# Optimization experiments

Hardware: AMD Instinct MI355X
Metric: run time of the kernel (lower is better)

The kernel has to match this reference:

```python
import jax, jax.numpy as jnp
import numpy as np
import math

N, T, V, D, DIN, H, L, F, MAXLEN = 8, 512, 32000, 512, 1024, 8, 2, 2048, 512
HD = D // H
STD = 0.02


def setup_inputs() -> dict:
    key = jax.random.key(0)
    ks = jax.random.split(key, 16)
    ln = jnp.stack([jnp.ones((L, D)), jnp.zeros((L, D))], axis=1)  # [L,2,D] (gamma, beta)
    return {
        "features": jax.random.normal(ks[0], (N, DIN), jnp.float32),
        "captions": jax.random.randint(ks[1], (N, T), 0, V, jnp.int32),
        "emb_table": jax.random.normal(ks[2], (V, D), jnp.float32) * STD,
        "pos_table": jax.random.normal(ks[3], (MAXLEN, D), jnp.float32) * STD,
        "feat_W": jax.random.normal(ks[4], (DIN, D), jnp.float32) * STD,
        "feat_b": jnp.zeros((D,), jnp.float32),
        "sa_qkv_W": jax.random.normal(ks[5], (L, 3, D, D), jnp.float32) * STD,
        "sa_qkv_b": jnp.zeros((L, 3, D), jnp.float32),
        "sa_o_W": jax.random.normal(ks[6], (L, D, D), jnp.float32) * STD,
        "sa_o_b": jnp.zeros((L, D), jnp.float32),
        "sa_ln": ln,
        "ca_qkv_W": jax.random.normal(ks[7], (L, 3, D, D), jnp.float32) * STD,
        "ca_qkv_b": jnp.zeros((L, 3, D), jnp.float32),
        "ca_o_W": jax.random.normal(ks[8], (L, D, D), jnp.float32) * STD,
        "ca_o_b": jnp.zeros((L, D), jnp.float32),
        "ca_ln": ln,
        "ff_W1": jax.random.normal(ks[9], (L, D, F), jnp.float32) * STD,
        "ff_b1": jnp.zeros((L, F), jnp.float32),
        "ff_W2": jax.random.normal(ks[10], (L, F, D), jnp.float32) * STD,
        "ff_b2": jnp.zeros((L, D), jnp.float32),
        "ff_ln": ln,
        "out_W": jax.random.normal(ks[11], (D, V), jnp.float32) * STD,
        "out_b": jnp.zeros((V,), jnp.float32),
    }


def layernorm(x, g, b, eps=1e-5):
    mu = jnp.mean(x, axis=-1, keepdims=True)
    var = jnp.mean(jnp.square(x - mu), axis=-1, keepdims=True)
    return (x - mu) * jax.lax.rsqrt(var + eps) * g + b


def mha(xq, xkv, Wqkv, bqkv, Wo, bo, mask):
    # xq: [N,Tq,D], xkv: [N,S,D]; heads split after separate q/k/v projections
    q = xq @ Wqkv[0] + bqkv[0]
    k = xkv @ Wqkv[1] + bqkv[1]
    v = xkv @ Wqkv[2] + bqkv[2]
    q = q.reshape(q.shape[0], q.shape[1], H, HD).transpose(0, 2, 1, 3)  # [N,H,Tq,hd]
    k = k.reshape(k.shape[0], k.shape[1], H, HD).transpose(0, 2, 1, 3)
    v = v.reshape(v.shape[0], v.shape[1], H, HD).transpose(0, 2, 1, 3)
    scores = jnp.einsum("nhtd,nhsd->nhts", q, k) / math.sqrt(HD)
    if mask is not None:
        scores = scores + jnp.where(mask == 0, -jnp.inf, 0.0)  # additive -inf mask
    attn = jax.nn.softmax(scores, axis=-1)  # dropout is identity in eval
    y = jnp.einsum("nhts,nhsd->nhtd", attn, v)
    y = y.transpose(0, 2, 1, 3).reshape(y.shape[0], -1, D)  # [N,Tq,D]
    return y @ Wo + bo


def reference(features, captions, emb_table, pos_table, feat_W, feat_b,
              sa_qkv_W, sa_qkv_b, sa_o_W, sa_o_b, sa_ln,
              ca_qkv_W, ca_qkv_b, ca_o_W, ca_o_b, ca_ln,
              ff_W1, ff_b1, ff_W2, ff_b2, ff_ln, out_W, out_b):
    cond = (features @ feat_W + feat_b)[:, None, :]  # [N,1,D]
    t = captions.shape[1]
    x = emb_table[captions] + pos_table[:t]  # token + positional embedding
    mask = jnp.tril(jnp.ones((t, t), jnp.float32))  # causal mask
    for l in range(L):
        a = mha(x, x, sa_qkv_W[l], sa_qkv_b[l], sa_o_W[l], sa_o_b[l], mask)
        x = layernorm(x + a, sa_ln[l, 0], sa_ln[l, 1])
        a = mha(x, cond, ca_qkv_W[l], ca_qkv_b[l], ca_o_W[l], ca_o_b[l], None)
        x = layernorm(x + a, ca_ln[l, 0], ca_ln[l, 1])
        h = jax.nn.relu(x @ ff_W1[l] + ff_b1[l]) @ ff_W2[l] + ff_b2[l]
        x = layernorm(x + h, ff_ln[l, 0], ff_ln[l, 1])
    return x @ out_W + out_b  # [N,T,V]
```

## Files before the change

### kernel.cpp

```cpp
#include <hip/hip_runtime.h>
#include <math.h>
#include <stdint.h>

#define N_ 8
#define T_ 512
#define V_ 32000
#define D_ 512
#define DIN_ 1024
#define H_ 8
#define HD_ 64
#define L_ 2
#define F_ 2048

typedef __attribute__((ext_vector_type(8))) short short8;
typedef __attribute__((ext_vector_type(4))) float f32x4;

__device__ __forceinline__ short f2bf(float f) {
  uint32_t u = __builtin_bit_cast(uint32_t, f);
  u = (u + 0x7FFFu + ((u >> 16) & 1u)) >> 16;
  return (short)u;
}
__device__ __forceinline__ uint32_t pack_bf2(float a, float b) {
  return (uint32_t)(uint16_t)f2bf(a) | ((uint32_t)(uint16_t)f2bf(b) << 16);
}
__device__ __forceinline__ float bflo(uint32_t u) {
  return __builtin_bit_cast(float, u << 16);
}
__device__ __forceinline__ float bfhi(uint32_t u) {
  return __builtin_bit_cast(float, u & 0xffff0000u);
}
__device__ __forceinline__ void unp8(uint4 p, float* v) {
  v[0] = bflo(p.x); v[1] = bfhi(p.x); v[2] = bflo(p.y); v[3] = bfhi(p.y);
  v[4] = bflo(p.z); v[5] = bfhi(p.z); v[6] = bflo(p.w); v[7] = bfhi(p.w);
}
__device__ __forceinline__ int swzb(int row, int byteoff) {
  return row * 128 + (byteoff ^ ((row & 7) << 4));
}

__global__ __launch_bounds__(256) void batched_transpose_kernel(
    const float* __restrict__ sa_qkv_W, const float* __restrict__ sa_o_W,
    const float* __restrict__ ff_W1, const float* __restrict__ ff_W2,
    const float* __restrict__ out_W, short* __restrict__ wq,
    short* __restrict__ wo, short* __restrict__ w1, short* __restrict__ w2,
    short* __restrict__ outWt) {
  __shared__ float tile[64][65];
  const int t = blockIdx.x;
  const float* src;
  short* dst;
  int K, N, rem;
  if (t < 384) {
    int mat = t >> 6;
    rem = t & 63;
    K = D_; N = D_;
    src = sa_qkv_W + (size_t)mat * D_ * D_;
    dst = wq + (size_t)mat * D_ * D_;
  } else if (t < 512) {
    int lt = t - 384, mat = lt >> 6;
    rem = lt & 63;
    K = D_; N = D_;
    src = sa_o_W + (size_t)mat * D_ * D_;
    dst = wo + (size_t)mat * D_ * D_;
  } else if (t < 1024) {
    int lt = t - 512, mat = lt >> 8;
    rem = lt & 255;
    K = D_; N = F_;
    src = ff_W1 + (size_t)mat * D_ * F_;
    dst = w1 + (size_t)mat * F_ * D_;
  } else if (t < 1536) {
    int lt = t - 1024, mat = lt >> 8;
    rem = lt & 255;
    K = F_; N = D_;
    src = ff_W2 + (size_t)mat * F_ * D_;
    dst = w2 + (size_t)mat * D_ * F_;
  } else {
    rem = t - 1536;
    K = D_; N = V_;
    src = out_W;
    dst = outWt;
  }
  const int nx = N >> 6;
  const int n0 = (rem % nx) * 64, k0 = (rem / nx) * 64;
  const int tid = threadIdx.x;
  const int c = tid & 63, r4 = tid >> 6;
#pragma unroll
  for (int i = 0; i < 16; ++i) {
    int k = r4 + i * 4;
    tile[k][c] = src[(size_t)(k0 + k) * N + n0 + c];
  }
  __syncthreads();
#pragma unroll
  for (int i = 0; i < 16; ++i) {
    int n = r4 + i * 4;
    dst[(size_t)(n0 + n) * K + k0 + c] = f2bf(tile[c][n]);
  }
}

template <int BM, int BN, bool RELU, bool OUTBF, int ORDER, bool NT>
__global__ __launch_bounds__((BM / 64) * (BN / 64) * 64) void bf16_gemm_kernel(
    const short* __restrict__ A, const short* __restrict__ Bt,
    const float* __restrict__ bias, void* __restrict__ Cv, int M, int N,
    int K) {
  constexpr int WM = BM / 64, WN = BN / 64, NW = WM * WN;
  constexpr int AISS = BM / (NW * 8), BISS = BN / (NW * 8);
  __shared__ short As[BM * 64];
  __shared__ short Bs[BN * 64];
  const int tid = threadIdx.x, lane = tid & 63, w = tid >> 6;
  const int wr = w / WN, wc = w % WN;
  const int lhi = lane >> 4, llo = lane & 15;

  const int gx = gridDim.x, gy = gridDim.y;
  const int nwg = gx * gy;
  int lin = blockIdx.y * gx + blockIdx.x;
  if ((nwg & 7) == 0) lin = (lin & 7) * (nwg >> 3) + (lin >> 3);
  int bm, bn;
  if (ORDER == 1) {
    bm = (lin % gy) * BM;
    bn = (lin / gy) * BN;
  } else {
    bm = (lin / gx) * BM;
    bn = (lin % gx) * BN;
  }

  const int arow = lane >> 3;
  const int achunk = ((lane & 7) ^ (lane >> 3)) * 8;

  f32x4 acc[4][4];
#pragma unroll
  for (int i = 0; i < 4; ++i)
#pragma unroll
    for (int j = 0; j < 4; ++j) acc[i][j] = (f32x4)0.f;

  char* AsB = (char*)As;
  char* BsB = (char*)Bs;

  for (int k0 = 0; k0 < K; k0 += 64) {
#pragma unroll
    for (int g = 0; g < AISS; ++g) {
      const int r0 = (w * AISS + g) * 8;
      const short* gp = A + (size_t)(bm + r0 + arow) * K + k0 + achunk;
      __builtin_amdgcn_global_load_lds(
          (const __attribute__((address_space(1))) void*)gp,
          (__attribute__((address_space(3))) void*)&As[r0 * 64], 16, 0, 0);
    }
#pragma unroll
    for (int g = 0; g < BISS; ++g) {
      const int r0 = (w * BISS + g) * 8;
      const short* gp = Bt + (size_t)(bn + r0 + arow) * K + k0 + achunk;
      __builtin_amdgcn_global_load_lds(
          (const __attribute__((address_space(1))) void*)gp,
          (__attribute__((address_space(3))) void*)&Bs[r0 * 64], 16, 0, 0);
    }
    __syncthreads();
#pragma unroll
    for (int ks = 0; ks < 2; ++ks) {
      short8 af[4], bf[4];
#pragma unroll
      for (int i = 0; i < 4; ++i)
        af[i] = *(const short8*)(AsB + swzb(wr * 64 + i * 16 + llo,
                                            ks * 64 + lhi * 16));
#pragma unroll
      for (int j = 0; j < 4; ++j)
        bf[j] = *(const short8*)(BsB + swzb(wc * 64 + j * 16 + llo,
                                            ks * 64 + lhi * 16));
#pragma unroll
      for (int i = 0; i < 4; ++i)
#pragma unroll
        for (int j = 0; j < 4; ++j)
          acc[i][j] = __builtin_amdgcn_mfma_f32_16x16x32_bf16(af[i], bf[j],
                                                              acc[i][j], 0, 0, 0);
    }
    __syncthreads();
  }
#pragma unroll
  for (int j = 0; j < 4; ++j) {
    const int col = bn + wc * 64 + j * 16 + llo;
    const float bv = bias ? bias[col] : 0.f;
#pragma unroll
    for (int i = 0; i < 4; ++i) {
      const int row0 = bm + wr * 64 + i * 16 + lhi * 4;
#pragma unroll
      for (int r = 0; r < 4; ++r) {
        float v = acc[i][j][r] + bv;
        if (RELU) v = fmaxf(v, 0.f);
        if (OUTBF) {
          ((short*)Cv)[(size_t)(row0 + r) * N + col] = f2bf(v);
        } else if (NT) {
          __builtin_nontemporal_store(v, &((float*)Cv)[(size_t)(row0 + r) * N + col]);
        } else {
          ((float*)Cv)[(size_t)(row0 + r) * N + col] = v;
        }
      }
    }
  }
}

template <int BM, int BN, int BK, int TM, int TN>
__global__ __launch_bounds__((BM / TM) * (BN / TN)) void gemm_f32_kernel(
    const short* __restrict__ A, const float* __restrict__ B,
    const float* __restrict__ bias, float* __restrict__ C, int M, int N,
    int K) {
  constexpr int THREADS = (BM / TM) * (BN / TN);
  __shared__ float As[BK][BM + 1];
  __shared__ float Bs[BK][BN + 1];
  const int tid = threadIdx.x;
  const int bm = blockIdx.y * BM, bn = blockIdx.x * BN;
  const int tcol = tid % (BN / TN), trow = tid / (BN / TN);
  float acc[TM][TN];
#pragma unroll
  for (int i = 0; i < TM; ++i)
#pragma unroll
    for (int j = 0; j < TN; ++j) acc[i][j] = 0.f;
  for (int k0 = 0; k0 < K; k0 += BK) {
    for (int i = tid; i < BM * BK; i += THREADS) {
      int m = i / BK, kk = i % BK;
      As[kk][m] = bflo((uint32_t)(uint16_t)A[(size_t)(bm + m) * K + (k0 + kk)]);
    }
    for (int i = tid; i < BK * BN; i += THREADS) {
      int kk = i / BN, n = i % BN;
      Bs[kk][n] = B[(size_t)(k0 + kk) * N + (bn + n)];
    }
    __syncthreads();
#pragma unroll
    for (int kk = 0; kk < BK; ++kk) {
      float a[TM], b[TN];
#pragma unroll
      for (int i = 0; i < TM; ++i) a[i] = As[kk][trow * TM + i];
#pragma unroll
      for (int j = 0; j < TN; ++j) b[j] = Bs[kk][tcol * TN + j];
#pragma unroll
      for (int i = 0; i < TM; ++i)
#pragma unroll
        for (int j = 0; j < TN; ++j) acc[i][j] += a[i] * b[j];
    }
    __syncthreads();
  }
#pragma unroll
  for (int i = 0; i < TM; ++i) {
    int m = bm + trow * TM + i;
#pragma unroll
    for (int j = 0; j < TN; ++j) {
      int n = bn + tcol * TN + j;
      C[(size_t)m * N + n] = acc[i][j] + (bias ? bias[n] : 0.f);
    }
  }
}

__global__ __launch_bounds__(256) void embed_kernel(
    const int* __restrict__ captions, const float* __restrict__ emb,
    const float* __restrict__ pos, short* __restrict__ xb) {
  int idx4 = (blockIdx.x * 256 + threadIdx.x) * 4;
  int d = idx4 % D_;
  int nt = idx4 / D_;
  int t = nt % T_;
  int tok = captions[nt];
  float4 e = *(const float4*)(emb + (size_t)tok * D_ + d);
  float4 p = *(const float4*)(pos + (size_t)t * D_ + d);
  *(uint32_t*)(xb + idx4) = pack_bf2(e.x + p.x, e.y + p.y);
  *(uint32_t*)(xb + idx4 + 2) = pack_bf2(e.z + p.z, e.w + p.w);
}

__global__ __launch_bounds__(256) void wave_mm_kernel(
    const float* __restrict__ A, const float* __restrict__ W,
    const float* __restrict__ bias, float* __restrict__ out, int M, int K,
    int N) {
  const int widx = blockIdx.x * 4 + (threadIdx.x >> 6);
  const int lane = threadIdx.x & 63;
  if (widx >= M * N) return;
  const int m = widx / N, n = widx % N;
  const float* a = A + (size_t)m * K;
  const float* w = W + n;
  float s = 0.f;
  for (int k = lane; k < K; k += 64) s += a[k] * w[(size_t)k * N];
#pragma unroll
  for (int off = 32; off; off >>= 1) s += __shfl_xor(s, off);
  if (lane == 0) out[widx] = s + (bias ? bias[n] : 0.f);
}

__global__ __launch_bounds__(256) void ca_mm_kernel(
    const float* __restrict__ A, size_t a_lstride, const float* __restrict__ W,
    size_t w_lstride, const float* __restrict__ bias, size_t b_lstride,
    float* __restrict__ out, int M, int K, int N) {
  const int widx = blockIdx.x * 4 + (threadIdx.x >> 6);
  const int lane = threadIdx.x & 63;
  if (widx >= L_ * M * N) return;
  const int l = widx / (M * N);
  const int r = widx % (M * N);
  const int m = r / N, n = r % N;
  const float* a = A + l * a_lstride + (size_t)m * K;
  const float* w = W + l * w_lstride + n;
  float s = 0.f;
  for (int k = lane; k < K; k += 64) s += a[k] * w[(size_t)k * N];
#pragma unroll
  for (int off = 32; off; off >>= 1) s += __shfl_xor(s, off);
  if (lane == 0) out[widx] = s + bias[l * b_lstride + n];
}

__global__ __launch_bounds__(256) void flash_attn_kernel(
    const short* __restrict__ qkv, short* __restrict__ y) {
  __shared__ short Ks[2][64 * 64];
  __shared__ short Vt[2][64 * 64];
  __shared__ short Ps[4][16 * 64];
  const int b = blockIdx.x;
  const int pair = b & 255, half = b >> 8;
  const int n = pair >> 5;
  const int h = (pair >> 2) & 7;
  const int tp = pair & 3;
  const int tile = half ? 7 - tp : tp;
  const int t0 = tile * 64;
  const int tid = threadIdx.x, lane = tid & 63, w = tid >> 6;
  const int lhi = lane >> 4, llo = lane & 15;
  char* PsB = (char*)Ps[w];

  const short* qrow = qkv + (size_t)(n * T_ + t0 + w * 16 + llo) * 1536 + h * 64;
  short8 qf[2];
#pragma unroll
  for (int kc = 0; kc < 2; ++kc) qf[kc] = *(const short8*)(qrow + kc * 32 + lhi * 8);

  float m = -1e30f, l = 0.f;
  f32x4 acc[4];
#pragma unroll
  for (int dc = 0; dc < 4; ++dc) acc[dc] = (f32x4)0.f;

  const int arow = lane >> 3;
  const int achunk = ((lane & 7) ^ (lane >> 3)) * 8;
  const int vr = tid >> 2, vd0 = (tid & 3) * 16;
  const int tg = t0 + w * 16 + llo;

  auto stageK = [&](int buf, int s0) {
#pragma unroll
    for (int g = 0; g < 2; ++g) {
      const int r0 = w * 16 + g * 8;
      const short* gp =
          qkv + (size_t)(n * T_ + s0 + r0 + arow) * 1536 + 512 + h * 64 + achunk;
      __builtin_amdgcn_global_load_lds(
          (const __attribute__((address_space(1))) void*)gp,
          (__attribute__((address_space(3))) void*)&Ks[buf][r0 * 64], 16, 0, 0);
    }
  };
  auto loadV = [&](int s0, short8& a, short8& bb) {
    const short* vg = qkv + (size_t)(n * T_ + s0 + vr) * 1536 + 1024 + h * 64 + vd0;
    a = *(const short8*)(vg);
    bb = *(const short8*)(vg + 8);
  };
  auto scatterV = [&](int buf, const short8& a, const short8& bb) {
    char* VtB = (char*)Vt[buf];
#pragma unroll
    for (int j = 0; j < 8; ++j) {
      *(short*)(VtB + swzb(vd0 + j, vr * 2)) = a[j];
      *(short*)(VtB + swzb(vd0 + 8 + j, vr * 2)) = bb[j];
    }
  };

  const int nchunk = tile + 1;
  {
    short8 va, vb;
    stageK(0, 0);
    loadV(0, va, vb);
    scatterV(0, va, vb);
  }
  __syncthreads();

  for (int c = 0; c < nchunk; ++c) {
    const int cur = c & 1;
    const int s0 = c * 64;
    short8 va, vb;
    const bool nxt = (c + 1 < nchunk);
    if (nxt) {
      stageK(cur ^ 1, s0 + 64);
      loadV(s0 + 64, va, vb);
    }
    char* KsB = (char*)Ks[cur];
    char* VtB = (char*)Vt[cur];

    f32x4 st[4];
    __builtin_amdgcn_s_setprio(1);
#pragma unroll
    for (int tle = 0; tle < 4; ++tle) {
      st[tle] = (f32x4)0.f;
#pragma unroll
      for (int kc = 0; kc < 2; ++kc) {
        short8 kf =
            *(const short8*)(KsB + swzb(tle * 16 + llo, kc * 64 + lhi * 16));
        st[tle] =
            __builtin_amdgcn_mfma_f32_16x16x32_bf16(kf, qf[kc], st[tle], 0, 0, 0);
      }
    }
    __builtin_amdgcn_s_setprio(0);
#pragma unroll
    for (int tle = 0; tle < 4; ++tle)
#pragma unroll
      for (int r = 0; r < 4; ++r) st[tle][r] *= 0.125f;
    if (s0 == t0) {
#pragma unroll
      for (int tle = 0; tle < 4; ++tle)
#pragma unroll
        for (int r = 0; r < 4; ++r)
          if (s0 + tle * 16 + lhi * 4 + r > tg) st[tle][r] = -1e30f;
    }
    float cmax = -1e30f;
#pragma unroll
    for (int tle = 0; tle < 4; ++tle)
#pragma unroll
      for (int r = 0; r < 4; ++r) cmax = fmaxf(cmax, st[tle][r]);
    cmax = fmaxf(cmax, __shfl_xor(cmax, 16));
    cmax = fmaxf(cmax, __shfl_xor(cmax, 32));
    float mn = fmaxf(m, cmax);
    float corr = __expf(m - mn);
    float lsum = 0.f;
#pragma unroll
    for (int tle = 0; tle < 4; ++tle)
#pragma unroll
      for (int r = 0; r < 4; ++r) {
        float p = __expf(st[tle][r] - mn);
        st[tle][r] = p;
        lsum += p;
      }
    lsum += __shfl_xor(lsum, 16);
    lsum += __shfl_xor(lsum, 32);
    l = l * corr + lsum;
    m = mn;
#pragma unroll
    for (int tle = 0; tle < 4; ++tle) {
      int base = swzb(llo, tle * 32 + lhi * 8);
      *(uint32_t*)(PsB + base) = pack_bf2(st[tle][0], st[tle][1]);
      *(uint32_t*)(PsB + base + 4) = pack_bf2(st[tle][2], st[tle][3]);
    }
    float c0 = __shfl(corr, lhi * 4 + 0), c1 = __shfl(corr, lhi * 4 + 1);
    float c2 = __shfl(corr, lhi * 4 + 2), c3 = __shfl(corr, lhi * 4 + 3);
#pragma unroll
    for (int dc = 0; dc < 4; ++dc) {
      acc[dc][0] *= c0;
      acc[dc][1] *= c1;
      acc[dc][2] *= c2;
      acc[dc][3] *= c3;
    }
    short8 pf0 = *(const short8*)(PsB + swzb(llo, lhi * 16));
    short8 pf1 = *(const short8*)(PsB + swzb(llo, 64 + lhi * 16));
    __builtin_amdgcn_s_setprio(1);
#pragma unroll
    for (int dc = 0; dc < 4; ++dc) {
      short8 vf0 = *(const short8*)(VtB + swzb(dc * 16 + llo, lhi * 16));
      short8 vf1 = *(const short8*)(VtB + swzb(dc * 16 + llo, 64 + lhi * 16));
      acc[dc] = __builtin_amdgcn_mfma_f32_16x16x32_bf16(pf0, vf0, acc[dc], 0, 0, 0);
      acc[dc] = __builtin_amdgcn_mfma_f32_16x16x32_bf16(pf1, vf1, acc[dc], 0, 0, 0);
    }
    __builtin_amdgcn_s_setprio(0);
    if (nxt) scatterV(cur ^ 1, va, vb);
    __syncthreads();
  }

  float linv = 1.f / l;
  float l0 = __shfl(linv, lhi * 4 + 0), l1 = __shfl(linv, lhi * 4 + 1);
  float l2 = __shfl(linv, lhi * 4 + 2), l3 = __shfl(linv, lhi * 4 + 3);
  short* yb = y + (size_t)(n * T_ + t0 + w * 16) * D_ + h * 64;
#pragma unroll
  for (int dc = 0; dc < 4; ++dc) {
    yb[(size_t)(lhi * 4 + 0) * D_ + dc * 16 + llo] = f2bf(acc[dc][0] * l0);
    yb[(size_t)(lhi * 4 + 1) * D_ + dc * 16 + llo] = f2bf(acc[dc][1] * l1);
    yb[(size_t)(lhi * 4 + 2) * D_ + dc * 16 + llo] = f2bf(acc[dc][2] * l2);
    yb[(size_t)(lhi * 4 + 3) * D_ + dc * 16 + llo] = f2bf(acc[dc][3] * l3);
  }
}

__global__ __launch_bounds__(256) void ln_res_kernel(
    short* __restrict__ xb, const short* __restrict__ res,
    const float* __restrict__ g, const float* __restrict__ b) {
  const int row = blockIdx.x * 4 + (threadIdx.x >> 6);
  const int lane = threadIdx.x & 63;
  const int d0 = lane * 8;
  uint4 xp = *(const uint4*)(xb + (size_t)row * D_ + d0);
  uint4 rp = *(const uint4*)(res + (size_t)row * D_ + d0);
  float xv[8], rv[8], v[8];
  unp8(xp, xv);
  unp8(rp, rv);
  float s = 0.f, sq = 0.f;
#pragma unroll
  for (int i = 0; i < 8; ++i) {
    v[i] = xv[i] + rv[i];
    s += v[i];
    sq += v[i] * v[i];
  }
#pragma unroll
  for (int off = 32; off; off >>= 1) {
    s += __shfl_xor(s, off);
    sq += __shfl_xor(sq, off);
  }
  float mu = s * (1.f / D_);
  float var = sq * (1.f / D_) - mu * mu;
  float r = rsqrtf(var + 1e-5f);
  float4 g0 = *(const float4*)(g + d0), g1 = *(const float4*)(g + d0 + 4);
  float4 b0 = *(const float4*)(b + d0), b1 = *(const float4*)(b + d0 + 4);
  float gg[8] = {g0.x, g0.y, g0.z, g0.w, g1.x, g1.y, g1.z, g1.w};
  float bb[8] = {b0.x, b0.y, b0.z, b0.w, b1.x, b1.y, b1.z, b1.w};
  float o[8];
#pragma unroll
  for (int i = 0; i < 8; ++i) o[i] = (v[i] - mu) * r * gg[i] + bb[i];
  uint4 op = {pack_bf2(o[0], o[1]), pack_bf2(o[2], o[3]),
              pack_bf2(o[4], o[5]), pack_bf2(o[6], o[7])};
  *(uint4*)(xb + (size_t)row * D_ + d0) = op;
}

__global__ __launch_bounds__(256) void ln2_res_kernel(
    short* __restrict__ xb, const short* __restrict__ res,
    const float* __restrict__ oc, const float* __restrict__ g1,
    const float* __restrict__ b1, const float* __restrict__ g2,
    const float* __restrict__ b2) {
  const int row = blockIdx.x * 4 + (threadIdx.x >> 6);
  const int lane = threadIdx.x & 63;
  const int d0 = lane * 8;
  uint4 xp = *(const uint4*)(xb + (size_t)row * D_ + d0);
  uint4 rp = *(const uint4*)(res + (size_t)row * D_ + d0);
  float xv[8], rv[8], v[8];
  unp8(xp, xv);
  unp8(rp, rv);
  float s = 0.f, sq = 0.f;
#pragma unroll
  for (int i = 0; i < 8; ++i) {
    v[i] = xv[i] + rv[i];
    s += v[i];
    sq += v[i] * v[i];
  }
#pragma unroll
  for (int off = 32; off; off >>= 1) {
    s += __shfl_xor(s, off);
    sq += __shfl_xor(sq, off);
  }
  float mu = s * (1.f / D_);
  float var = sq * (1.f / D_) - mu * mu;
  float r = rsqrtf(var + 1e-5f);
  float4 ga = *(const float4*)(g1 + d0), gb = *(const float4*)(g1 + d0 + 4);
  float4 ba = *(const float4*)(b1 + d0), bbv = *(const float4*)(b1 + d0 + 4);
  const float* ocr = oc + (size_t)(row / T_) * D_ + d0;
  float4 oa = *(const float4*)(ocr), ob = *(const float4*)(ocr + 4);
  float g1v[8] = {ga.x, ga.y, ga.z, ga.w, gb.x, gb.y, gb.z, gb.w};
  float b1v[8] = {ba.x, ba.y, ba.z, ba.w, bbv.x, bbv.y, bbv.z, bbv.w};
  float ov[8] = {oa.x, oa.y, oa.z, oa.w, ob.x, ob.y, ob.z, ob.w};
  float u[8];
  float s2 = 0.f, sq2 = 0.f;
#pragma unroll
  for (int i = 0; i < 8; ++i) {
    u[i] = (v[i] - mu) * r * g1v[i] + b1v[i] + ov[i];
    s2 += u[i];
    sq2 += u[i] * u[i];
  }
#pragma unroll
  for (int off = 32; off; off >>= 1) {
    s2 += __shfl_xor(s2, off);
    sq2 += __shfl_xor(sq2, off);
  }
  float mu2 = s2 * (1.f / D_);
  float var2 = sq2 * (1.f / D_) - mu2 * mu2;
  float r2 = rsqrtf(var2 + 1e-5f);
  float4 gc = *(const float4*)(g2 + d0), gd = *(const float4*)(g2 + d0 + 4);
  float4 bc = *(const float4*)(b2 + d0), bd = *(const float4*)(b2 + d0 + 4);
  float g2v[8] = {gc.x, gc.y, gc.z, gc.w, gd.x, gd.y, gd.z, gd.w};
  float b2v[8] = {bc.x, bc.y, bc.z, bc.w, bd.x, bd.y, bd.z, bd.w};
  float o[8];
#pragma unroll
  for (int i = 0; i < 8; ++i) o[i] = (u[i] - mu2) * r2 * g2v[i] + b2v[i];
  uint4 op = {pack_bf2(o[0], o[1]), pack_bf2(o[2], o[3]),
              pack_bf2(o[4], o[5]), pack_bf2(o[6], o[7])};
  *(uint4*)(xb + (size_t)row * D_ + d0) = op;
}

extern "C" void kernel_launch(void* const* d_in, const int* in_sizes, int n_in,
                              void* d_out, int out_size, void* d_ws,
                              size_t ws_size, hipStream_t stream) {
  const float* features = (const float*)d_in[0];
  const int* captions = (const int*)d_in[1];
  const float* emb_table = (const float*)d_in[2];
  const float* pos_table = (const float*)d_in[3];
  const float* feat_W = (const float*)d_in[4];
  const float* feat_b = (const float*)d_in[5];
  const float* sa_qkv_W = (const float*)d_in[6];
  const float* sa_qkv_b = (const float*)d_in[7];
  const float* sa_o_W = (const float*)d_in[8];
  const float* sa_o_b = (const float*)d_in[9];
  const float* sa_ln = (const float*)d_in[10];
  const float* ca_qkv_W = (const float*)d_in[11];
  const float* ca_qkv_b = (const float*)d_in[12];
  const float* ca_o_W = (const float*)d_in[13];
  const float* ca_o_b = (const float*)d_in[14];
  const float* ca_ln = (const float*)d_in[15];
  const float* ff_W1 = (const float*)d_in[16];
  const float* ff_b1 = (const float*)d_in[17];
  const float* ff_W2 = (const float*)d_in[18];
  const float* ff_b2 = (const float*)d_in[19];
  const float* ff_ln = (const float*)d_in[20];
  const float* out_W = (const float*)d_in[21];
  const float* out_b = (const float*)d_in[22];

  const int ROWS = N_ * T_;
  float* out = (float*)d_out;

  short* xb = (short*)d_ws;
  float* cond = (float*)(xb + (size_t)ROWS * D_);
  float* vcAll = cond + N_ * D_;
  float* ocAll = vcAll + (size_t)L_ * N_ * D_;
  short* outWt = (short*)(ocAll + (size_t)L_ * N_ * D_);
  size_t ws_need = (size_t)ROWS * D_ * 2 + (1 + 2 * L_) * N_ * D_ * 4 +
                   (size_t)V_ * D_ * 2;
  const bool big_ws = ws_size >= ws_need;

  short* qkvb = (short*)out;
  short* yb = qkvb + (size_t)ROWS * 3 * D_;
  short* ffhb = yb + (size_t)ROWS * D_;
  short* tmpb = ffhb + (size_t)ROWS * F_;
  short* wq = tmpb + (size_t)ROWS * D_;
  short* wo = wq + (size_t)L_ * 3 * D_ * D_;
  short* w1 = wo + (size_t)L_ * D_ * D_;
  short* w2 = w1 + (size_t)L_ * F_ * D_;

  hipLaunchKernelGGL(batched_transpose_kernel, dim3(big_ws ? 5536 : 1536),
                     dim3(256), 0, stream, sa_qkv_W, sa_o_W, ff_W1, ff_W2,
                     out_W, wq, wo, w1, w2, outWt);

  auto mg128 = [&](const short* A, const short* Bt, const float* bias, void* C,
                   int M, int Nn, int K, bool relu) {
    dim3 grid(Nn / 128, M / 128);
    if (relu)
      hipLaunchKernelGGL((bf16_gemm_kernel<128, 128, true, true, 0, false>),
                         grid, dim3(256), 0, stream, A, Bt, bias, C, M, Nn, K);
    else
      hipLaunchKernelGGL((bf16_gemm_kernel<128, 128, false, true, 0, false>),
                         grid, dim3(256), 0, stream, A, Bt, bias, C, M, Nn, K);
  };
  auto mg64 = [&](const short* A, const short* Bt, const float* bias, void* C,
                  int M, int Nn, int K) {
    dim3 grid(Nn / 128, M / 64);
    hipLaunchKernelGGL((bf16_gemm_kernel<64, 128, false, true, 0, false>),
                       grid, dim3(128), 0, stream, A, Bt, bias, C, M, Nn, K);
  };

  hipLaunchKernelGGL(wave_mm_kernel, dim3((N_ * D_ + 3) / 4), dim3(256), 0,
                     stream, features, feat_W, feat_b, cond, N_, DIN_, D_);
  hipLaunchKernelGGL(ca_mm_kernel, dim3((L_ * N_ * D_ + 3) / 4), dim3(256), 0,
                     stream, cond, (size_t)0, ca_qkv_W + (size_t)2 * D_ * D_,
                     (size_t)3 * D_ * D_, ca_qkv_b + 2 * D_, (size_t)3 * D_,
                     vcAll, N_, D_, D_);
  hipLaunchKernelGGL(ca_mm_kernel, dim3((L_ * N_ * D_ + 3) / 4), dim3(256), 0,
                     stream, vcAll, (size_t)N_ * D_, ca_o_W, (size_t)D_ * D_,
                     ca_o_b, (size_t)D_, ocAll, N_, D_, D_);
  hipLaunchKernelGGL(embed_kernel, dim3(ROWS * D_ / 1024), dim3(256), 0, stream,
                     captions, emb_table, pos_table, xb);

  for (int l = 0; l < L_; ++l) {
    mg128(xb, wq + (size_t)l * 3 * D_ * D_, sa_qkv_b + (size_t)l * 3 * D_,
          qkvb, ROWS, 3 * D_, D_, false);
    hipLaunchKernelGGL(flash_attn_kernel, dim3(512), dim3(256), 0, stream,
                       qkvb, yb);
    mg64(yb, wo + (size_t)l * D_ * D_, sa_o_b + (size_t)l * D_, tmpb, ROWS, D_,
         D_);
    hipLaunchKernelGGL(ln2_res_kernel, dim3(ROWS / 4), dim3(256), 0, stream,
                       xb, tmpb, ocAll + (size_t)l * N_ * D_,
                       sa_ln + (size_t)l * 2 * D_,
                       sa_ln + (size_t)l * 2 * D_ + D_,
                       ca_ln + (size_t)l * 2 * D_,
                       ca_ln + (size_t)l * 2 * D_ + D_);

    mg128(xb, w1 + (size_t)l * F_ * D_, ff_b1 + (size_t)l * F_, ffhb, ROWS, F_,
          D_, true);
    mg64(ffhb, w2 + (size_t)l * D_ * F_, ff_b2 + (size_t)l * D_, tmpb, ROWS,
         D_, F_);
    hipLaunchKernelGGL(ln_res_kernel, dim3(ROWS / 4), dim3(256), 0, stream, xb,
                       tmpb, ff_ln + (size_t)l * 2 * D_,
                       ff_ln + (size_t)l * 2 * D_ + D_);
  }

  if (big_ws) {
    dim3 grid(V_ / 128, ROWS / 128);
    hipLaunchKernelGGL((bf16_gemm_kernel<128, 128, false, false, 1, true>),
                       grid, dim3(256), 0, stream, xb, outWt, out_b, out, ROWS,
                       V_, D_);
  } else {
    dim3 grid(V_ / 64, ROWS / 128);
    hipLaunchKernelGGL((gemm_f32_kernel<128, 64, 16, 8, 4>), grid, dim3(256), 0,
                       stream, xb, out_W, out_b, out, ROWS, V_, D_);
  }
}
```

Baseline: 470.1 us.

## Fold softmax scale into QKV GEMM, lazy rescale in flash attention, compile-time K

Makes K a template parameter of the bf16 GEMM so its loop trip count and strides are known at compile time. The 1/sqrt(hd) scale is applied to the Q columns in the QKV GEMM epilogue, which removes the per-tile score scaling in attention. Flash attention now skips the running-max update and accumulator rescale when the new tile max exceeds the old one by at most 8 for every lane in the wave. Skipping the update risks larger exponent values, and scaling Q before the bf16 rounding changes rounding slightly.

Measured after the change: 500.5 us. +6.5%, slower.

```diff
diff --git a/kernel.cpp b/kernel.cpp
--- a/kernel.cpp
+++ b/kernel.cpp
@@ -95,11 +95,11 @@
   }
 }
 
-template <int BM, int BN, bool RELU, bool OUTBF, int ORDER, bool NT>
+template <int BM, int BN, int KT, bool RELU, bool OUTBF, bool QS, int ORDER,
+          bool NT>
 __global__ __launch_bounds__((BM / 64) * (BN / 64) * 64) void bf16_gemm_kernel(
     const short* __restrict__ A, const short* __restrict__ Bt,
-    const float* __restrict__ bias, void* __restrict__ Cv, int M, int N,
-    int K) {
+    const float* __restrict__ bias, void* __restrict__ Cv, int M, int N) {
   constexpr int WM = BM / 64, WN = BN / 64, NW = WM * WN;
   constexpr int AISS = BM / (NW * 8), BISS = BN / (NW * 8);
   __shared__ short As[BM * 64];
@@ -133,11 +133,11 @@
   char* AsB = (char*)As;
   char* BsB = (char*)Bs;
 
-  for (int k0 = 0; k0 < K; k0 += 64) {
+  for (int k0 = 0; k0 < KT; k0 += 64) {
 #pragma unroll
     for (int g = 0; g < AISS; ++g) {
       const int r0 = (w * AISS + g) * 8;
-      const short* gp = A + (size_t)(bm + r0 + arow) * K + k0 + achunk;
+      const short* gp = A + (size_t)(bm + r0 + arow) * KT + k0 + achunk;
       __builtin_amdgcn_global_load_lds(
           (const __attribute__((address_space(1))) void*)gp,
           (__attribute__((address_space(3))) void*)&As[r0 * 64], 16, 0, 0);
@@ -145,7 +145,7 @@
 #pragma unroll
     for (int g = 0; g < BISS; ++g) {
       const int r0 = (w * BISS + g) * 8;
-      const short* gp = Bt + (size_t)(bn + r0 + arow) * K + k0 + achunk;
+      const short* gp = Bt + (size_t)(bn + r0 + arow) * KT + k0 + achunk;
       __builtin_amdgcn_global_load_lds(
           (const __attribute__((address_space(1))) void*)gp,
           (__attribute__((address_space(3))) void*)&Bs[r0 * 64], 16, 0, 0);
@@ -175,6 +175,7 @@
   for (int j = 0; j < 4; ++j) {
     const int col = bn + wc * 64 + j * 16 + llo;
     const float bv = bias ? bias[col] : 0.f;
+    const float scl = (QS && col < 512) ? 0.125f : 1.f;
 #pragma unroll
     for (int i = 0; i < 4; ++i) {
       const int row0 = bm + wr * 64 + i * 16 + lhi * 4;
@@ -182,6 +183,7 @@
       for (int r = 0; r < 4; ++r) {
         float v = acc[i][j][r] + bv;
         if (RELU) v = fmaxf(v, 0.f);
+        if (QS) v *= scl;
         if (OUTBF) {
           ((short*)Cv)[(size_t)(row0 + r) * N + col] = f2bf(v);
         } else if (NT) {
@@ -386,10 +388,6 @@
       }
     }
     __builtin_amdgcn_s_setprio(0);
-#pragma unroll
-    for (int tle = 0; tle < 4; ++tle)
-#pragma unroll
-      for (int r = 0; r < 4; ++r) st[tle][r] *= 0.125f;
     if (s0 == t0) {
 #pragma unroll
       for (int tle = 0; tle < 4; ++tle)
@@ -404,8 +402,8 @@
       for (int r = 0; r < 4; ++r) cmax = fmaxf(cmax, st[tle][r]);
     cmax = fmaxf(cmax, __shfl_xor(cmax, 16));
     cmax = fmaxf(cmax, __shfl_xor(cmax, 32));
-    float mn = fmaxf(m, cmax);
-    float corr = __expf(m - mn);
+    const bool skip = __all(cmax - m <= 8.f);
+    float mn = skip ? m : fmaxf(m, cmax);
     float lsum = 0.f;
 #pragma unroll
     for (int tle = 0; tle < 4; ++tle)
@@ -417,22 +415,27 @@
       }
     lsum += __shfl_xor(lsum, 16);
     lsum += __shfl_xor(lsum, 32);
-    l = l * corr + lsum;
-    m = mn;
 #pragma unroll
     for (int tle = 0; tle < 4; ++tle) {
       int base = swzb(llo, tle * 32 + lhi * 8);
       *(uint32_t*)(PsB + base) = pack_bf2(st[tle][0], st[tle][1]);
       *(uint32_t*)(PsB + base + 4) = pack_bf2(st[tle][2], st[tle][3]);
     }
-    float c0 = __shfl(corr, lhi * 4 + 0), c1 = __shfl(corr, lhi * 4 + 1);
-    float c2 = __shfl(corr, lhi * 4 + 2), c3 = __shfl(corr, lhi * 4 + 3);
-#pragma unroll
-    for (int dc = 0; dc < 4; ++dc) {
-      acc[dc][0] *= c0;
-      acc[dc][1] *= c1;
-      acc[dc][2] *= c2;
-      acc[dc][3] *= c3;
+    if (skip) {
+      l = l + lsum;
+    } else {
+      float corr = __expf(m - mn);
+      l = l * corr + lsum;
+      m = mn;
+      float c0 = __shfl(corr, lhi * 4 + 0), c1 = __shfl(corr, lhi * 4 + 1);
+      float c2 = __shfl(corr, lhi * 4 + 2), c3 = __shfl(corr, lhi * 4 + 3);
+#pragma unroll
+      for (int dc = 0; dc < 4; ++dc) {
+        acc[dc][0] *= c0;
+        acc[dc][1] *= c1;
+        acc[dc][2] *= c2;
+        acc[dc][3] *= c3;
+      }
     }
     short8 pf0 = *(const short8*)(PsB + swzb(llo, lhi * 16));
     short8 pf1 = *(const short8*)(PsB + swzb(llo, 64 + lhi * 16));
@@ -615,23 +618,6 @@
                      dim3(256), 0, stream, sa_qkv_W, sa_o_W, ff_W1, ff_W2,
                      out_W, wq, wo, w1, w2, outWt);
 
-  auto mg128 = [&](const short* A, const short* Bt, const float* bias, void* C,
-                   int M, int Nn, int K, bool relu) {
-    dim3 grid(Nn / 128, M / 128);
-    if (relu)
-      hipLaunchKernelGGL((bf16_gemm_kernel<128, 128, true, true, 0, false>),
-                         grid, dim3(256), 0, stream, A, Bt, bias, C, M, Nn, K);
-    else
-      hipLaunchKernelGGL((bf16_gemm_kernel<128, 128, false, true, 0, false>),
-                         grid, dim3(256), 0, stream, A, Bt, bias, C, M, Nn, K);
-  };
-  auto mg64 = [&](const short* A, const short* Bt, const float* bias, void* C,
-                  int M, int Nn, int K) {
-    dim3 grid(Nn / 128, M / 64);
-    hipLaunchKernelGGL((bf16_gemm_kernel<64, 128, false, true, 0, false>),
-                       grid, dim3(128), 0, stream, A, Bt, bias, C, M, Nn, K);
-  };
-
   hipLaunchKernelGGL(wave_mm_kernel, dim3((N_ * D_ + 3) / 4), dim3(256), 0,
                      stream, features, feat_W, feat_b, cond, N_, DIN_, D_);
   hipLaunchKernelGGL(ca_mm_kernel, dim3((L_ * N_ * D_ + 3) / 4), dim3(256), 0,
@@ -645,12 +631,17 @@
                      captions, emb_table, pos_table, xb);
 
   for (int l = 0; l < L_; ++l) {
-    mg128(xb, wq + (size_t)l * 3 * D_ * D_, sa_qkv_b + (size_t)l * 3 * D_,
-          qkvb, ROWS, 3 * D_, D_, false);
+    hipLaunchKernelGGL(
+        (bf16_gemm_kernel<128, 128, 512, false, true, true, 0, false>),
+        dim3(3 * D_ / 128, ROWS / 128), dim3(256), 0, stream, xb,
+        wq + (size_t)l * 3 * D_ * D_, sa_qkv_b + (size_t)l * 3 * D_, qkvb,
+        ROWS, 3 * D_);
     hipLaunchKernelGGL(flash_attn_kernel, dim3(512), dim3(256), 0, stream,
                        qkvb, yb);
-    mg64(yb, wo + (size_t)l * D_ * D_, sa_o_b + (size_t)l * D_, tmpb, ROWS, D_,
-         D_);
+    hipLaunchKernelGGL(
+        (bf16_gemm_kernel<64, 128, 512, false, true, false, 0, false>),
+        dim3(D_ / 128, ROWS / 64), dim3(128), 0, stream, yb,
+        wo + (size_t)l * D_ * D_, sa_o_b + (size_t)l * D_, tmpb, ROWS, D_);
     hipLaunchKernelGGL(ln2_res_kernel, dim3(ROWS / 4), dim3(256), 0, stream,
                        xb, tmpb, ocAll + (size_t)l * N_ * D_,
                        sa_ln + (size_t)l * 2 * D_,
@@ -658,20 +649,24 @@
                        ca_ln + (size_t)l * 2 * D_,
                        ca_ln + (size_t)l * 2 * D_ + D_);
 
-    mg128(xb, w1 + (size_t)l * F_ * D_, ff_b1 + (size_t)l * F_, ffhb, ROWS, F_,
-          D_, true);
-    mg64(ffhb, w2 + (size_t)l * D_ * F_, ff_b2 + (size_t)l * D_, tmpb, ROWS,
-         D_, F_);
+    hipLaunchKernelGGL(
+        (bf16_gemm_kernel<128, 128, 512, true, true, false, 0, false>),
+        dim3(F_ / 128, ROWS / 128), dim3(256), 0, stream, xb,
+        w1 + (size_t)l * F_ * D_, ff_b1 + (size_t)l * F_, ffhb, ROWS, F_);
+    hipLaunchKernelGGL(
+        (bf16_gemm_kernel<64, 128, 2048, false, true, false, 0, false>),
+        dim3(D_ / 128, ROWS / 64), dim3(128), 0, stream, ffhb,
+        w2 + (size_t)l * D_ * F_, ff_b2 + (size_t)l * D_, tmpb, ROWS, D_);
     hipLaunchKernelGGL(ln_res_kernel, dim3(ROWS / 4), dim3(256), 0, stream, xb,
                        tmpb, ff_ln + (size_t)l * 2 * D_,
                        ff_ln + (size_t)l * 2 * D_ + D_);
   }
 
   if (big_ws) {
-    dim3 grid(V_ / 128, ROWS / 128);
-    hipLaunchKernelGGL((bf16_gemm_kernel<128, 128, false, false, 1, true>),
-                       grid, dim3(256), 0, stream, xb, outWt, out_b, out, ROWS,
-                       V_, D_);
+    hipLaunchKernelGGL(
+        (bf16_gemm_kernel<128, 128, 512, false, false, false, 1, true>),
+        dim3(V_ / 128, ROWS / 128), dim3(256), 0, stream, xb, outWt, out_b,
+        out, ROWS, V_);
   } else {
     dim3 grid(V_ / 64, ROWS / 128);
     hipLaunchKernelGGL((gemm_f32_kernel<128, 64, 16, 8, 4>), grid, dim3(256), 0,
```
